# Performance work log

Hardware: AMD Instinct MI355X
Metric: run time of the kernel (lower is better)

The kernel has to match this reference:

```python
import jax, jax.numpy as jnp
import numpy as np

S, D_IN, D = 4, 1024, 256   # n_scales, input dim, d_per_scale (d_model=1024)
B, T = 4, 4096
R_MIN, R_MAX, TH_MIN, TH_MAX = 0.9, 0.999, 0.01, 1.0


def setup_inputs() -> dict:
    key = jax.random.key(0)
    ks = jax.random.split(key, 6)
    s_in = 1.0 / np.sqrt(D_IN)
    s_h = 1.0 / np.sqrt(D)
    return {
        'x':   jax.random.normal(ks[0], (B, T, D_IN), jnp.float32),
        'Wg1': jax.random.normal(ks[1], (S, D_IN, D), jnp.float32) * s_in,
        'bg1': jnp.zeros((S, D), jnp.float32),
        'Wg2': jax.random.normal(ks[2], (S, D, D), jnp.float32) * s_h,
        'bg2': jnp.full((S, D), -4.0, jnp.float32),  # bias_init=constant(-4.0)
        'Wdr': jax.random.normal(ks[3], (S, D_IN, D), jnp.float32) * s_in,
        'bdr': jnp.zeros((S, D), jnp.float32),
        'Wdi': jax.random.normal(ks[4], (S, D_IN, D), jnp.float32) * s_in,
        'bdi': jnp.zeros((S, D), jnp.float32),
    }


def _scale_consts():
    r = np.concatenate([[1.0], np.linspace(R_MAX, R_MIN, S - 1)])
    theta = np.concatenate([[0.0], np.linspace(TH_MIN, TH_MAX, S - 1)])
    a_base = (r * np.exp(1j * theta)).astype(np.complex64)        # (S,)
    bscale = np.where(r >= 1.0, 1.0 / np.sqrt(D), 1.0 - r).astype(np.float32)  # (S,)
    return jnp.asarray(a_base), jnp.asarray(bscale)


def reference(x, Wg1, bg1, Wg2, bg2, Wdr, bdr, Wdi, bdi):
    a_base, bscale = _scale_consts()
    # gate MLP (conditioning = x): (B,S,T,D)
    g1 = jax.nn.relu(jnp.einsum('bti,sid->bstd', x, Wg1) + bg1[None, :, None, :])
    gate = jax.nn.sigmoid(jnp.einsum('bstd,sde->bste', g1, Wg2) + bg2[None, :, None, :])
    # complex drive
    dre = jnp.einsum('bti,sid->bstd', x, Wdr) + bdr[None, :, None, :]
    dim = jnp.einsum('bti,sid->bstd', x, Wdi) + bdi[None, :, None, :]
    omg = (1.0 - gate).astype(jnp.complex64)                       # (B,S,T,D)
    a = omg * a_base[None, :, None, None]
    b = omg * ((dre + 1j * dim).astype(jnp.complex64) * bscale[None, :, None, None])
    # linear recurrence h_t = a_t*h_{t-1} + b_t via associative scan along time
    def binop(left, right):
        al, bl = left
        ar, br = right
        return (al * ar, ar * bl + br)
    _, h = jax.lax.associative_scan(binop, (a, b), axis=2)         # (B,S,T,D)
    h = jnp.moveaxis(h, 1, 2)                                      # (B,T,S,D)
    out = jnp.stack([h.real, h.imag], axis=3)                      # (B,T,S,2,D) -> re/im per scale
    return out.reshape(B, T, S * 2 * D)
```

## Files before the change

### kernel.cpp

```cpp
#include <hip/hip_runtime.h>
#include <cmath>

#define S_   4
#define DIN  1024
#define D_   256
#define B_   4
#define T_   4096
#define BT_  (B_*T_)
#define GN   (S_*3*D_)
#define CHUNKS 128
#define CL   (T_/CHUNKS)

typedef short bf16x8 __attribute__((ext_vector_type(8)));
typedef float f32x4  __attribute__((ext_vector_type(4)));

struct SC { float are[S_]; float aim[S_]; float bsc[S_]; };

__device__ inline unsigned short f2bf(float f) {
    unsigned int u = __builtin_bit_cast(unsigned int, f);
    unsigned int r = (u + 0x7FFFu + ((u >> 16) & 1u)) >> 16;
    return (unsigned short)r;
}

#define GLD_LDS(gp, lp) \
    __builtin_amdgcn_global_load_lds( \
        (const __attribute__((address_space(1))) void*)(gp), \
        (__attribute__((address_space(3))) void*)(lp), 16, 0, 0)

__global__ __launch_bounds__(256) void kconv_x(
    const float* __restrict__ x, unsigned short* __restrict__ xb)
{
    const size_t i = ((size_t)blockIdx.x*256 + threadIdx.x)*4;
    const float4 v = *(const float4*)(x + i);
    ushort4 o;
    o.x = f2bf(v.x); o.y = f2bf(v.y); o.z = f2bf(v.z); o.w = f2bf(v.w);
    *(ushort4*)(xb + i) = o;
}

__global__ __launch_bounds__(256) void kconv_w(
    const float* __restrict__ src, unsigned short* __restrict__ dst,
    int K, int N, size_t dst_s_stride)
{
    __shared__ float t[32][33];
    const int k0 = blockIdx.x*32, n0 = blockIdx.y*32, s = blockIdx.z;
    const float* sp = src + (size_t)s*K*N;
    unsigned short* dp = dst + (size_t)s*dst_s_stride;
    const int c = threadIdx.x & 31, r0 = threadIdx.x >> 5;
    #pragma unroll
    for (int p = 0; p < 4; ++p)
        t[r0 + p*8][c] = sp[(size_t)(k0 + r0 + p*8)*N + n0 + c];
    __syncthreads();
    #pragma unroll
    for (int p = 0; p < 4; ++p)
        dp[(size_t)(n0 + r0 + p*8)*K + k0 + c] = f2bf(t[c][r0 + p*8]);
}

__global__ __launch_bounds__(256) void k1_mfma(
    const unsigned short* __restrict__ xb,
    const unsigned short* __restrict__ Bct,
    const float* __restrict__ bg1, const float* __restrict__ bdr,
    const float* __restrict__ bdi,
    unsigned short* __restrict__ g1b, float* __restrict__ out)
{
    __shared__ unsigned short As[128*64];
    __shared__ unsigned short Bs[128*64];

    const int tid = threadIdx.x;
    const int wave = tid >> 6, lane = tid & 63;
    const int wm = (wave >> 1) * 64, wn = (wave & 1) * 64;
    const int row0 = blockIdx.x * 128, col0 = blockIdx.y * 128;

    const f32x4 z = {0.f, 0.f, 0.f, 0.f};
    f32x4 acc[4][4];
    #pragma unroll
    for (int i = 0; i < 4; ++i)
        #pragma unroll
        for (int j = 0; j < 4; ++j) acc[i][j] = z;

    const unsigned short* Ag = xb  + (size_t)row0*DIN;
    const unsigned short* Bg = Bct + (size_t)col0*DIN;
    const int lrow = lane >> 3;
    const int lk   = (lane & 7) * 8;
    const int cn   = lane & 15, quad = lane >> 4;

    for (int k0 = 0; k0 < DIN; k0 += 64) {
        #pragma unroll
        for (int t = 0; t < 4; ++t) {
            const int m0 = wave*32 + t*8;
            GLD_LDS(Ag + (size_t)(m0 + lrow)*DIN + k0 + lk, As + m0*64);
            GLD_LDS(Bg + (size_t)(m0 + lrow)*DIN + k0 + lk, Bs + m0*64);
        }
        __syncthreads();
        #pragma unroll
        for (int ks = 0; ks < 2; ++ks) {
            const int kb = ks*32 + quad*8;
            bf16x8 af[4], bfv[4];
            #pragma unroll
            for (int i = 0; i < 4; ++i)
                af[i] = *(const bf16x8*)(As + (wm + i*16 + cn)*64 + kb);
            #pragma unroll
            for (int j = 0; j < 4; ++j)
                bfv[j] = *(const bf16x8*)(Bs + (wn + j*16 + cn)*64 + kb);
            #pragma unroll
            for (int i = 0; i < 4; ++i)
                #pragma unroll
                for (int j = 0; j < 4; ++j)
                    acc[i][j] = __builtin_amdgcn_mfma_f32_16x16x32_bf16(
                        af[i], bfv[j], acc[i][j], 0, 0, 0);
        }
        __syncthreads();
    }

    const int s    = col0 / 768;
    const int rem  = col0 - s*768;
    const int mat  = rem >> 8;
    const int dbase = (rem & 255) + wn + cn;
    const float* bias = (mat == 0) ? bg1 : ((mat == 1) ? bdr : bdi);
    float bv[4];
    #pragma unroll
    for (int j = 0; j < 4; ++j) bv[j] = bias[s*D_ + dbase + j*16];

    const int qr = quad * 4;
    #pragma unroll
    for (int i = 0; i < 4; ++i) {
        const int m = row0 + wm + i*16 + qr;
        #pragma unroll
        for (int j = 0; j < 4; ++j) {
            const int d = dbase + j*16;
            const f32x4 v = acc[i][j];
            if (mat == 0) {
                unsigned short* gp = g1b + ((size_t)s*BT_ + m)*D_ + d;
                #pragma unroll
                for (int r = 0; r < 4; ++r)
                    gp[(size_t)r*D_] = f2bf(fmaxf(v[r] + bv[j], 0.f));
            } else {
                float* op = out + (size_t)m*(S_*2*D_) + s*2*D_
                          + (mat == 2 ? D_ : 0) + d;
                #pragma unroll
                for (int r = 0; r < 4; ++r)
                    op[(size_t)r*(S_*2*D_)] = v[r] + bv[j];
            }
        }
    }
}

__global__ __launch_bounds__(256) void k2_mfma(
    const unsigned short* __restrict__ g1b,
    const unsigned short* __restrict__ B2t,
    const float* __restrict__ bg2, float* __restrict__ omg)
{
    __shared__ unsigned short As[128*64];
    __shared__ unsigned short Bs[128*64];

    const int tid = threadIdx.x;
    const int wave = tid >> 6, lane = tid & 63;
    const int wm = (wave >> 1) * 64, wn = (wave & 1) * 64;
    const int row0 = blockIdx.x * 128, col0 = blockIdx.y * 128;
    const int s = blockIdx.z;

    const f32x4 z = {0.f, 0.f, 0.f, 0.f};
    f32x4 acc[4][4];
    #pragma unroll
    for (int i = 0; i < 4; ++i)
        #pragma unroll
        for (int j = 0; j < 4; ++j) acc[i][j] = z;

    const unsigned short* Ag = g1b + ((size_t)s*BT_ + row0)*D_;
    const unsigned short* Bg = B2t + (size_t)s*D_*D_ + (size_t)col0*D_;
    const int lrow = lane >> 3;
    const int lk   = (lane & 7) * 8;
    const int cn   = lane & 15, quad = lane >> 4;

    for (int k0 = 0; k0 < D_; k0 += 64) {
        #pragma unroll
        for (int t = 0; t < 4; ++t) {
            const int m0 = wave*32 + t*8;
            GLD_LDS(Ag + (size_t)(m0 + lrow)*D_ + k0 + lk, As + m0*64);
            GLD_LDS(Bg + (size_t)(m0 + lrow)*D_ + k0 + lk, Bs + m0*64);
        }
        __syncthreads();
        #pragma unroll
        for (int ks = 0; ks < 2; ++ks) {
            const int kb = ks*32 + quad*8;
            bf16x8 af[4], bfv[4];
            #pragma unroll
            for (int i = 0; i < 4; ++i)
                af[i] = *(const bf16x8*)(As + (wm + i*16 + cn)*64 + kb);
            #pragma unroll
            for (int j = 0; j < 4; ++j)
                bfv[j] = *(const bf16x8*)(Bs + (wn + j*16 + cn)*64 + kb);
            #pragma unroll
            for (int i = 0; i < 4; ++i)
                #pragma unroll
                for (int j = 0; j < 4; ++j)
                    acc[i][j] = __builtin_amdgcn_mfma_f32_16x16x32_bf16(
                        af[i], bfv[j], acc[i][j], 0, 0, 0);
        }
        __syncthreads();
    }

    const int qr = quad * 4;
    float bv[4];
    #pragma unroll
    for (int j = 0; j < 4; ++j) bv[j] = bg2[s*D_ + col0 + wn + j*16 + cn];

    #pragma unroll
    for (int i = 0; i < 4; ++i) {
        const int m = row0 + wm + i*16 + qr;
        #pragma unroll
        for (int j = 0; j < 4; ++j) {
            const int d = col0 + wn + j*16 + cn;
            const f32x4 v = acc[i][j];
            float* op = omg + ((size_t)s*BT_ + m)*D_ + d;
            #pragma unroll
            for (int r = 0; r < 4; ++r)
                op[(size_t)r*D_] = 1.f / (1.f + __expf(v[r] + bv[j]));
        }
    }
}

__global__ __launch_bounds__(256) void k3a_chunk(
    const float* __restrict__ omg, const float* __restrict__ out,
    float4* __restrict__ summ, SC sc)
{
    const int blk = blockIdx.x;
    const int c = blk & (CHUNKS-1);
    const int s = (blk / CHUNKS) & (S_-1);
    const int b = blk / (CHUNKS*S_);
    const int d = threadIdx.x;

    const float are = sc.are[s], aim = sc.aim[s], bs = sc.bsc[s];
    float Ar = 1.f, Ai = 0.f, Hr = 0.f, Hi = 0.f;
    const int t0 = c * CL;

    #pragma unroll 4
    for (int t = 0; t < CL; ++t) {
        const int bt = b*T_ + t0 + t;
        const float om = omg[((size_t)s*BT_ + bt)*D_ + d];
        const float* op = out + (size_t)bt*(S_*2*D_) + s*2*D_;
        const float dre = op[d], dim = op[D_ + d];
        const float ar = om*are, ai = om*aim;
        const float ob = om*bs;
        const float br = ob*dre, bi = ob*dim;
        const float nHr = ar*Hr - ai*Hi + br;
        const float nHi = ar*Hi + ai*Hr + bi;
        const float nAr = ar*Ar - ai*Ai;
        const float nAi = ar*Ai + ai*Ar;
        Hr = nHr; Hi = nHi; Ar = nAr; Ai = nAi;
    }
    summ[((size_t)(b*S_ + s)*CHUNKS + c)*D_ + d] = make_float4(Ar, Ai, Hr, Hi);
}

__global__ __launch_bounds__(256) void k3b_scan(float4* __restrict__ summ)
{
    const int idx = blockIdx.x*256 + threadIdx.x;
    const int d = idx & (D_-1);
    const int s = (idx >> 8) & (S_-1);
    const int b = idx >> 10;

    float cr = 0.f, ci = 0.f;
    for (int c = 0; c < CHUNKS; ++c) {
        const size_t off = ((size_t)(b*S_ + s)*CHUNKS + c)*D_ + d;
        const float4 v = summ[off];
        const float ncr = v.x*cr - v.y*ci + v.z;
        const float nci = v.x*ci + v.y*cr + v.w;
        *(float2*)&summ[off] = make_float2(cr, ci);
        cr = ncr; ci = nci;
    }
}

__global__ __launch_bounds__(256) void k3c_final(
    const float* __restrict__ omg, float* __restrict__ out,
    const float4* __restrict__ summ, SC sc)
{
    const int blk = blockIdx.x;
    const int c = blk & (CHUNKS-1);
    const int s = (blk / CHUNKS) & (S_-1);
    const int b = blk / (CHUNKS*S_);
    const int d = threadIdx.x;

    const float are = sc.are[s], aim = sc.aim[s], bs = sc.bsc[s];
    const float4 v = summ[((size_t)(b*S_ + s)*CHUNKS + c)*D_ + d];
    float Hr = v.x, Hi = v.y;
    const int t0 = c * CL;

    #pragma unroll 4
    for (int t = 0; t < CL; ++t) {
        const int bt = b*T_ + t0 + t;
        const float om = omg[((size_t)s*BT_ + bt)*D_ + d];
        float* op = out + (size_t)bt*(S_*2*D_) + s*2*D_;
        const float dre = op[d], dim = op[D_ + d];
        const float ar = om*are, ai = om*aim;
        const float ob = om*bs;
        const float br = ob*dre, bi = ob*dim;
        const float nHr = ar*Hr - ai*Hi + br;
        const float nHi = ar*Hi + ai*Hr + bi;
        Hr = nHr; Hi = nHi;
        op[d]      = Hr;
        op[D_ + d] = Hi;
    }
}

extern "C" void kernel_launch(void* const* d_in, const int* in_sizes, int n_in,
                              void* d_out, int out_size, void* d_ws, size_t ws_size,
                              hipStream_t stream)
{
    const float* x   = (const float*)d_in[0];
    const float* Wg1 = (const float*)d_in[1];
    const float* bg1 = (const float*)d_in[2];
    const float* Wg2 = (const float*)d_in[3];
    const float* bg2 = (const float*)d_in[4];
    const float* Wdr = (const float*)d_in[5];
    const float* bdr = (const float*)d_in[6];
    const float* Wdi = (const float*)d_in[7];
    const float* bdi = (const float*)d_in[8];
    float* out = (float*)d_out;

    char* ws = (char*)d_ws;
    float4*         summ = (float4*)ws;
    float*          omg  = (float*)(ws + 33554432);
    unsigned short* xb   = (unsigned short*)omg;
    unsigned short* g1b  = (unsigned short*)(ws + 33554432 + 67108864);
    unsigned short* Bct  = g1b + (size_t)S_*BT_*D_;
    unsigned short* B2t  = Bct + (size_t)GN*DIN;

    SC sc;
    {
        const double r[S_]  = {1.0, 0.999, 0.9495, 0.9};
        const double th[S_] = {0.0, 0.01, 0.505, 1.0};
        for (int s = 0; s < S_; ++s) {
            sc.are[s] = (float)(r[s] * cos(th[s]));
            sc.aim[s] = (float)(r[s] * sin(th[s]));
            sc.bsc[s] = (r[s] >= 1.0) ? (float)(1.0/16.0) : (float)(1.0 - r[s]);
        }
    }

    kconv_x<<<(BT_*DIN)/1024, 256, 0, stream>>>(x, xb);
    kconv_w<<<dim3(32,8,S_), 256, 0, stream>>>(Wg1, Bct + 0*D_*DIN, DIN, D_, (size_t)768*DIN);
    kconv_w<<<dim3(32,8,S_), 256, 0, stream>>>(Wdr, Bct + 1*D_*DIN, DIN, D_, (size_t)768*DIN);
    kconv_w<<<dim3(32,8,S_), 256, 0, stream>>>(Wdi, Bct + 2*D_*DIN, DIN, D_, (size_t)768*DIN);
    kconv_w<<<dim3(8,8,S_),  256, 0, stream>>>(Wg2, B2t, D_, D_, (size_t)D_*D_);

    k1_mfma<<<dim3(BT_/128, GN/128), 256, 0, stream>>>(xb, Bct, bg1, bdr, bdi, g1b, out);
    k2_mfma<<<dim3(BT_/128, D_/128, S_), 256, 0, stream>>>(g1b, B2t, bg2, omg);

    k3a_chunk<<<B_*S_*CHUNKS, 256, 0, stream>>>(omg, out, summ, sc);
    k3b_scan <<<(B_*S_*D_)/256, 256, 0, stream>>>(summ);
    k3c_final<<<B_*S_*CHUNKS, 256, 0, stream>>>(omg, out, summ, sc);
}
```

Measured before the change: 473.7 us.

## Store gate and drive in 16-bit, swizzle GEMM LDS, vectorize scan two-wide

Stores the gate complement as 16-bit fixed point and, when the workspace is large enough, the complex drive as bf16 in a separate buffer instead of fp32 in the output. This cuts memory traffic in the two scan passes. Adds an XOR swizzle to the LDS tile layout of both GEMMs to avoid bank conflicts, and makes each scan thread handle two adjacent channels with vector loads. The workspace layout is reorganised with aliasing between buffers, and the lower precision of gate and drive adds error to the long recurrence.

```diff
diff --git a/kernel.cpp b/kernel.cpp
--- a/kernel.cpp
+++ b/kernel.cpp
@@ -21,6 +21,15 @@
     unsigned int r = (u + 0x7FFFu + ((u >> 16) & 1u)) >> 16;
     return (unsigned short)r;
 }
+__device__ inline float bf2f_lo(unsigned int u) {
+    return __builtin_bit_cast(float, u << 16);
+}
+__device__ inline float bf2f_hi(unsigned int u) {
+    return __builtin_bit_cast(float, u & 0xFFFF0000u);
+}
+__device__ inline float u16om(unsigned int u) {
+    return ((float)u + 0.5f) * (1.f/65536.f);
+}
 
 #define GLD_LDS(gp, lp) \
     __builtin_amdgcn_global_load_lds( \
@@ -55,12 +64,14 @@
         dp[(size_t)(n0 + r0 + p*8)*K + k0 + c] = f2bf(t[c][r0 + p*8]);
 }
 
+template<bool DRVB>
 __global__ __launch_bounds__(256) void k1_mfma(
     const unsigned short* __restrict__ xb,
     const unsigned short* __restrict__ Bct,
     const float* __restrict__ bg1, const float* __restrict__ bdr,
     const float* __restrict__ bdi,
-    unsigned short* __restrict__ g1b, float* __restrict__ out)
+    unsigned short* __restrict__ g1b,
+    unsigned short* __restrict__ drvb, float* __restrict__ drvf)
 {
     __shared__ unsigned short As[128*64];
     __shared__ unsigned short Bs[128*64];
@@ -80,27 +91,28 @@
     const unsigned short* Ag = xb  + (size_t)row0*DIN;
     const unsigned short* Bg = Bct + (size_t)col0*DIN;
     const int lrow = lane >> 3;
-    const int lk   = (lane & 7) * 8;
+    const int lksw = ((lane & 7) ^ lrow) * 8;
     const int cn   = lane & 15, quad = lane >> 4;
+    const int e    = cn & 7;
 
     for (int k0 = 0; k0 < DIN; k0 += 64) {
         #pragma unroll
         for (int t = 0; t < 4; ++t) {
             const int m0 = wave*32 + t*8;
-            GLD_LDS(Ag + (size_t)(m0 + lrow)*DIN + k0 + lk, As + m0*64);
-            GLD_LDS(Bg + (size_t)(m0 + lrow)*DIN + k0 + lk, Bs + m0*64);
+            GLD_LDS(Ag + (size_t)(m0 + lrow)*DIN + k0 + lksw, As + m0*64);
+            GLD_LDS(Bg + (size_t)(m0 + lrow)*DIN + k0 + lksw, Bs + m0*64);
         }
         __syncthreads();
         #pragma unroll
         for (int ks = 0; ks < 2; ++ks) {
-            const int kb = ks*32 + quad*8;
+            const int offs = (((ks*4 + quad) ^ e)) * 8;
             bf16x8 af[4], bfv[4];
             #pragma unroll
             for (int i = 0; i < 4; ++i)
-                af[i] = *(const bf16x8*)(As + (wm + i*16 + cn)*64 + kb);
+                af[i] = *(const bf16x8*)(As + (wm + i*16 + cn)*64 + offs);
             #pragma unroll
             for (int j = 0; j < 4; ++j)
-                bfv[j] = *(const bf16x8*)(Bs + (wn + j*16 + cn)*64 + kb);
+                bfv[j] = *(const bf16x8*)(Bs + (wn + j*16 + cn)*64 + offs);
             #pragma unroll
             for (int i = 0; i < 4; ++i)
                 #pragma unroll
@@ -134,11 +146,17 @@
                 for (int r = 0; r < 4; ++r)
                     gp[(size_t)r*D_] = f2bf(fmaxf(v[r] + bv[j], 0.f));
             } else {
-                float* op = out + (size_t)m*(S_*2*D_) + s*2*D_
-                          + (mat == 2 ? D_ : 0) + d;
-                #pragma unroll
-                for (int r = 0; r < 4; ++r)
-                    op[(size_t)r*(S_*2*D_)] = v[r] + bv[j];
+                const size_t base = (size_t)m*(S_*2*D_) + s*2*D_
+                                  + (mat == 2 ? D_ : 0) + d;
+                if (DRVB) {
+                    #pragma unroll
+                    for (int r = 0; r < 4; ++r)
+                        drvb[base + (size_t)r*(S_*2*D_)] = f2bf(v[r] + bv[j]);
+                } else {
+                    #pragma unroll
+                    for (int r = 0; r < 4; ++r)
+                        drvf[base + (size_t)r*(S_*2*D_)] = v[r] + bv[j];
+                }
             }
         }
     }
@@ -147,7 +165,7 @@
 __global__ __launch_bounds__(256) void k2_mfma(
     const unsigned short* __restrict__ g1b,
     const unsigned short* __restrict__ B2t,
-    const float* __restrict__ bg2, float* __restrict__ omg)
+    const float* __restrict__ bg2, unsigned short* __restrict__ omgu)
 {
     __shared__ unsigned short As[128*64];
     __shared__ unsigned short Bs[128*64];
@@ -168,27 +186,28 @@
     const unsigned short* Ag = g1b + ((size_t)s*BT_ + row0)*D_;
     const unsigned short* Bg = B2t + (size_t)s*D_*D_ + (size_t)col0*D_;
     const int lrow = lane >> 3;
-    const int lk   = (lane & 7) * 8;
+    const int lksw = ((lane & 7) ^ lrow) * 8;
     const int cn   = lane & 15, quad = lane >> 4;
+    const int e    = cn & 7;
 
     for (int k0 = 0; k0 < D_; k0 += 64) {
         #pragma unroll
         for (int t = 0; t < 4; ++t) {
             const int m0 = wave*32 + t*8;
-            GLD_LDS(Ag + (size_t)(m0 + lrow)*D_ + k0 + lk, As + m0*64);
-            GLD_LDS(Bg + (size_t)(m0 + lrow)*D_ + k0 + lk, Bs + m0*64);
+            GLD_LDS(Ag + (size_t)(m0 + lrow)*D_ + k0 + lksw, As + m0*64);
+            GLD_LDS(Bg + (size_t)(m0 + lrow)*D_ + k0 + lksw, Bs + m0*64);
         }
         __syncthreads();
         #pragma unroll
         for (int ks = 0; ks < 2; ++ks) {
-            const int kb = ks*32 + quad*8;
+            const int offs = (((ks*4 + quad) ^ e)) * 8;
             bf16x8 af[4], bfv[4];
             #pragma unroll
             for (int i = 0; i < 4; ++i)
-                af[i] = *(const bf16x8*)(As + (wm + i*16 + cn)*64 + kb);
+                af[i] = *(const bf16x8*)(As + (wm + i*16 + cn)*64 + offs);
             #pragma unroll
             for (int j = 0; j < 4; ++j)
-                bfv[j] = *(const bf16x8*)(Bs + (wn + j*16 + cn)*64 + kb);
+                bfv[j] = *(const bf16x8*)(Bs + (wn + j*16 + cn)*64 + offs);
             #pragma unroll
             for (int i = 0; i < 4; ++i)
                 #pragma unroll
@@ -211,44 +230,65 @@
         for (int j = 0; j < 4; ++j) {
             const int d = col0 + wn + j*16 + cn;
             const f32x4 v = acc[i][j];
-            float* op = omg + ((size_t)s*BT_ + m)*D_ + d;
-            #pragma unroll
-            for (int r = 0; r < 4; ++r)
-                op[(size_t)r*D_] = 1.f / (1.f + __expf(v[r] + bv[j]));
-        }
-    }
-}
-
-__global__ __launch_bounds__(256) void k3a_chunk(
-    const float* __restrict__ omg, const float* __restrict__ out,
+            unsigned short* op = omgu + ((size_t)s*BT_ + m)*D_ + d;
+            #pragma unroll
+            for (int r = 0; r < 4; ++r) {
+                const float om = 1.f / (1.f + __expf(v[r] + bv[j]));
+                op[(size_t)r*D_] =
+                    (unsigned short)fminf(om * 65536.f, 65535.f);
+            }
+        }
+    }
+}
+
+template<bool DRVB>
+__global__ __launch_bounds__(128) void k3a_chunk(
+    const unsigned short* __restrict__ omgu,
+    const unsigned short* __restrict__ drvb, const float* __restrict__ drvf,
     float4* __restrict__ summ, SC sc)
 {
     const int blk = blockIdx.x;
     const int c = blk & (CHUNKS-1);
-    const int s = (blk / CHUNKS) & (S_-1);
-    const int b = blk / (CHUNKS*S_);
-    const int d = threadIdx.x;
+    const int s = (blk >> 7) & (S_-1);
+    const int b = blk >> 9;
+    const int d2 = threadIdx.x;
 
     const float are = sc.are[s], aim = sc.aim[s], bs = sc.bsc[s];
-    float Ar = 1.f, Ai = 0.f, Hr = 0.f, Hi = 0.f;
+    float Ar[2] = {1.f,1.f}, Ai[2] = {0,0}, Hr[2] = {0,0}, Hi[2] = {0,0};
     const int t0 = c * CL;
 
     #pragma unroll 4
     for (int t = 0; t < CL; ++t) {
         const int bt = b*T_ + t0 + t;
-        const float om = omg[((size_t)s*BT_ + bt)*D_ + d];
-        const float* op = out + (size_t)bt*(S_*2*D_) + s*2*D_;
-        const float dre = op[d], dim = op[D_ + d];
-        const float ar = om*are, ai = om*aim;
-        const float ob = om*bs;
-        const float br = ob*dre, bi = ob*dim;
-        const float nHr = ar*Hr - ai*Hi + br;
-        const float nHi = ar*Hi + ai*Hr + bi;
-        const float nAr = ar*Ar - ai*Ai;
-        const float nAi = ar*Ai + ai*Ar;
-        Hr = nHr; Hi = nHi; Ar = nAr; Ai = nAi;
-    }
-    summ[((size_t)(b*S_ + s)*CHUNKS + c)*D_ + d] = make_float4(Ar, Ai, Hr, Hi);
+        const unsigned int ov =
+            *(const unsigned int*)(omgu + ((size_t)s*BT_ + bt)*D_ + 2*d2);
+        const float om[2] = { u16om(ov & 0xFFFFu), u16om(ov >> 16) };
+        const size_t base = (size_t)bt*(S_*2*D_) + s*2*D_ + 2*d2;
+        float dre[2], dim[2];
+        if (DRVB) {
+            const unsigned int ur = *(const unsigned int*)(drvb + base);
+            const unsigned int ui = *(const unsigned int*)(drvb + base + D_);
+            dre[0] = bf2f_lo(ur); dre[1] = bf2f_hi(ur);
+            dim[0] = bf2f_lo(ui); dim[1] = bf2f_hi(ui);
+        } else {
+            const float2 fr = *(const float2*)(drvf + base);
+            const float2 fi = *(const float2*)(drvf + base + D_);
+            dre[0] = fr.x; dre[1] = fr.y; dim[0] = fi.x; dim[1] = fi.y;
+        }
+        #pragma unroll
+        for (int u = 0; u < 2; ++u) {
+            const float ar = om[u]*are, ai = om[u]*aim, ob = om[u]*bs;
+            const float br = ob*dre[u], bi = ob*dim[u];
+            const float nHr = ar*Hr[u] - ai*Hi[u] + br;
+            const float nHi = ar*Hi[u] + ai*Hr[u] + bi;
+            const float nAr = ar*Ar[u] - ai*Ai[u];
+            const float nAi = ar*Ai[u] + ai*Ar[u];
+            Hr[u]=nHr; Hi[u]=nHi; Ar[u]=nAr; Ai[u]=nAi;
+        }
+    }
+    const size_t so = ((size_t)(b*S_ + s)*CHUNKS + c)*D_ + 2*d2;
+    summ[so]     = make_float4(Ar[0], Ai[0], Hr[0], Hi[0]);
+    summ[so + 1] = make_float4(Ar[1], Ai[1], Hr[1], Hi[1]);
 }
 
 __global__ __launch_bounds__(256) void k3b_scan(float4* __restrict__ summ)
@@ -269,35 +309,53 @@
     }
 }
 
-__global__ __launch_bounds__(256) void k3c_final(
-    const float* __restrict__ omg, float* __restrict__ out,
-    const float4* __restrict__ summ, SC sc)
+template<bool DRVB>
+__global__ __launch_bounds__(128) void k3c_final(
+    const unsigned short* __restrict__ omgu,
+    const unsigned short* __restrict__ drvb, const float* __restrict__ drvf,
+    float* __restrict__ out, const float4* __restrict__ summ, SC sc)
 {
     const int blk = blockIdx.x;
     const int c = blk & (CHUNKS-1);
-    const int s = (blk / CHUNKS) & (S_-1);
-    const int b = blk / (CHUNKS*S_);
-    const int d = threadIdx.x;
+    const int s = (blk >> 7) & (S_-1);
+    const int b = blk >> 9;
+    const int d2 = threadIdx.x;
 
     const float are = sc.are[s], aim = sc.aim[s], bs = sc.bsc[s];
-    const float4 v = summ[((size_t)(b*S_ + s)*CHUNKS + c)*D_ + d];
-    float Hr = v.x, Hi = v.y;
+    const size_t so = ((size_t)(b*S_ + s)*CHUNKS + c)*D_ + 2*d2;
+    const float4 v0 = summ[so];
+    const float4 v1 = summ[so + 1];
+    float Hr[2] = {v0.x, v1.x}, Hi[2] = {v0.y, v1.y};
     const int t0 = c * CL;
 
     #pragma unroll 4
     for (int t = 0; t < CL; ++t) {
         const int bt = b*T_ + t0 + t;
-        const float om = omg[((size_t)s*BT_ + bt)*D_ + d];
-        float* op = out + (size_t)bt*(S_*2*D_) + s*2*D_;
-        const float dre = op[d], dim = op[D_ + d];
-        const float ar = om*are, ai = om*aim;
-        const float ob = om*bs;
-        const float br = ob*dre, bi = ob*dim;
-        const float nHr = ar*Hr - ai*Hi + br;
-        const float nHi = ar*Hi + ai*Hr + bi;
-        Hr = nHr; Hi = nHi;
-        op[d]      = Hr;
-        op[D_ + d] = Hi;
+        const unsigned int ov =
+            *(const unsigned int*)(omgu + ((size_t)s*BT_ + bt)*D_ + 2*d2);
+        const float om[2] = { u16om(ov & 0xFFFFu), u16om(ov >> 16) };
+        const size_t base = (size_t)bt*(S_*2*D_) + s*2*D_ + 2*d2;
+        float dre[2], dim[2];
+        if (DRVB) {
+            const unsigned int ur = *(const unsigned int*)(drvb + base);
+            const unsigned int ui = *(const unsigned int*)(drvb + base + D_);
+            dre[0] = bf2f_lo(ur); dre[1] = bf2f_hi(ur);
+            dim[0] = bf2f_lo(ui); dim[1] = bf2f_hi(ui);
+        } else {
+            const float2 fr = *(const float2*)(drvf + base);
+            const float2 fi = *(const float2*)(drvf + base + D_);
+            dre[0] = fr.x; dre[1] = fr.y; dim[0] = fi.x; dim[1] = fi.y;
+        }
+        #pragma unroll
+        for (int u = 0; u < 2; ++u) {
+            const float ar = om[u]*are, ai = om[u]*aim, ob = om[u]*bs;
+            const float br = ob*dre[u], bi = ob*dim[u];
+            const float nHr = ar*Hr[u] - ai*Hi[u] + br;
+            const float nHi = ar*Hi[u] + ai*Hr[u] + bi;
+            Hr[u]=nHr; Hi[u]=nHi;
+        }
+        *(float2*)(out + base)      = make_float2(Hr[0], Hr[1]);
+        *(float2*)(out + base + D_) = make_float2(Hi[0], Hi[1]);
     }
 }
 
@@ -317,12 +375,14 @@
     float* out = (float*)d_out;
 
     char* ws = (char*)d_ws;
-    float4*         summ = (float4*)ws;
-    float*          omg  = (float*)(ws + 33554432);
-    unsigned short* xb   = (unsigned short*)omg;
-    unsigned short* g1b  = (unsigned short*)(ws + 33554432 + 67108864);
-    unsigned short* Bct  = g1b + (size_t)S_*BT_*D_;
-    unsigned short* B2t  = Bct + (size_t)GN*DIN;
+    unsigned short* g1b  = (unsigned short*)(ws + 0);
+    float4*         summ = (float4*)(ws + 0);
+    unsigned short* B2t  = (unsigned short*)(ws + 33554432);
+    unsigned short* xb   = (unsigned short*)(ws + 34078720);
+    unsigned short* omgu = (unsigned short*)(ws + 34078720);
+    unsigned short* Bct  = (unsigned short*)(ws + 67633152);
+    unsigned short* drvb = (unsigned short*)(ws + 73924608);
+    const bool drv_bf16 = ws_size >= (size_t)73924608 + 67108864;
 
     SC sc;
     {
@@ -341,10 +401,21 @@
     kconv_w<<<dim3(32,8,S_), 256, 0, stream>>>(Wdi, Bct + 2*D_*DIN, DIN, D_, (size_t)768*DIN);
     kconv_w<<<dim3(8,8,S_),  256, 0, stream>>>(Wg2, B2t, D_, D_, (size_t)D_*D_);
 
-    k1_mfma<<<dim3(BT_/128, GN/128), 256, 0, stream>>>(xb, Bct, bg1, bdr, bdi, g1b, out);
-    k2_mfma<<<dim3(BT_/128, D_/128, S_), 256, 0, stream>>>(g1b, B2t, bg2, omg);
-
-    k3a_chunk<<<B_*S_*CHUNKS, 256, 0, stream>>>(omg, out, summ, sc);
-    k3b_scan <<<(B_*S_*D_)/256, 256, 0, stream>>>(summ);
-    k3c_final<<<B_*S_*CHUNKS, 256, 0, stream>>>(omg, out, summ, sc);
-}
+    if (drv_bf16)
+        k1_mfma<true><<<dim3(BT_/128, GN/128), 256, 0, stream>>>(
+            xb, Bct, bg1, bdr, bdi, g1b, drvb, out);
+    else
+        k1_mfma<false><<<dim3(BT_/128, GN/128), 256, 0, stream>>>(
+            xb, Bct, bg1, bdr, bdi, g1b, drvb, out);
+    k2_mfma<<<dim3(BT_/128, D_/128, S_), 256, 0, stream>>>(g1b, B2t, bg2, omgu);
+
+    if (drv_bf16) {
+        k3a_chunk<true><<<B_*S_*CHUNKS, 128, 0, stream>>>(omgu, drvb, out, summ, sc);
+        k3b_scan       <<<(B_*S_*D_)/256, 256, 0, stream>>>(summ);
+        k3c_final<true><<<B_*S_*CHUNKS, 128, 0, stream>>>(omgu, drvb, out, out, summ, sc);
+    } else {
+        k3a_chunk<false><<<B_*S_*CHUNKS, 128, 0, stream>>>(omgu, drvb, out, summ, sc);
+        k3b_scan        <<<(B_*S_*D_)/256, 256, 0, stream>>>(summ);
+        k3c_final<false><<<B_*S_*CHUNKS, 128, 0, stream>>>(omgu, drvb, out, out, summ, sc);
+    }
+}
```

Measured after the change: 437.4 us. 7.7% less time.
